# Optimization experiments

Measured on AMD Instinct MI355X. Metric: run time of the kernel, lower is better.

Reference implementation:

```python
import jax, jax.numpy as jnp
import numpy as np

B, S, D, H = 8, 2048, 256, 4
DH = D // H
DFF = 4 * D


def setup_inputs() -> dict:
    key = jax.random.key(0)
    ks = jax.random.split(key, 32)
    w = lambda k, sh: (jax.random.normal(k, sh, jnp.float32) * 0.02)
    inp = {
        'global_feat': jax.random.normal(ks[0], (B, S, D), jnp.float32),
        'local_feat': jax.random.normal(ks[1], (B, S, D), jnp.float32),
        'text_feat': jax.random.normal(ks[2], (B, S, D), jnp.float32),
        'Wl1': w(ks[3], (D, D)), 'bl1': jnp.zeros((D,), jnp.float32),
        'Wl2': w(ks[4], (D, D)), 'bl2': jnp.zeros((D,), jnp.float32),
        'Wg': w(ks[5], (D, D)), 'bg': jnp.zeros((D,), jnp.float32),
        'Wgq': w(ks[6], (D, D)), 'bgq': jnp.zeros((D,), jnp.float32),
        'Wgk': w(ks[7], (D, D)), 'bgk': jnp.zeros((D,), jnp.float32),
        'Wgv': w(ks[8], (D, D)), 'bgv': jnp.zeros((D,), jnp.float32),
        'Wpq': w(ks[9], (D, D)), 'bpq': jnp.zeros((D,), jnp.float32),
        'Wpk': w(ks[10], (D, D)), 'bpk': jnp.zeros((D,), jnp.float32),
        'Wpv': w(ks[11], (D, D)), 'bpv': jnp.zeros((D,), jnp.float32),
        'Wd': w(ks[12], (D, D)), 'bd': jnp.zeros((D,), jnp.float32),
        'Wm1': w(ks[13], (D, DFF)), 'bm1': jnp.zeros((DFF,), jnp.float32),
        'Wm2': w(ks[14], (DFF, D)), 'bm2': jnp.zeros((D,), jnp.float32),
        'Wml': w(ks[15], (D, D)), 'bml': jnp.zeros((D,), jnp.float32),
    }
    return inp


def _heads(x):
    # [B,S,D] -> [B,H,S,DH]
    return x.reshape(B, S, H, DH).transpose(0, 2, 1, 3)


def _merge(x):
    # [B,H,S,DH] -> [B,S,D]
    return x.transpose(0, 2, 1, 3).reshape(B, S, D)


def reference(global_feat, local_feat, text_feat,
              Wl1, bl1, Wl2, bl2, Wg, bg,
              Wgq, bgq, Wgk, bgk, Wgv, bgv,
              Wpq, bpq, Wpk, bpk, Wpv, bpv,
              Wd, bd, Wm1, bm1, Wm2, bm2, Wml, bml):
    scale = 1.0 / jnp.sqrt(jnp.asarray(DH, jnp.float32))
    # embedding projections (dropout inactive in eval mode)
    dup_local = local_feat @ Wl1 + bl1      # local_embedding_1
    local = local_feat @ Wl2 + bl2          # local_embedding_2
    glob = global_feat @ Wg + bg            # global_embedding
    # global branch: Q from global, K/V from local
    gq = _heads(glob @ Wgq + bgq)
    gk = _heads(local @ Wgk + bgk)
    gv = _heads(local @ Wgv + bgv)
    # local branch: Q from duplicate local, K/V from text
    pq = _heads(dup_local @ Wpq + bpq)
    pk = _heads(text_feat @ Wpk + bpk)
    pv = _heads(text_feat @ Wpv + bpv)
    glb_probs = jax.nn.softmax(jnp.einsum('bhqd,bhkd->bhqk', gq, gk) * scale, axis=-1)
    plb_probs = jax.nn.softmax(jnp.einsum('bhqd,bhkd->bhqk', pq, pk) * scale, axis=-1)
    # bridging matmul: fuse probability maps
    plb_enhanced = jnp.einsum('bhqk,bhkl->bhql', glb_probs, plb_probs)
    glb_ctx = _merge(jnp.einsum('bhqk,bhkd->bhqd', glb_probs, gv))
    plb_ctx = _merge(jnp.einsum('bhqk,bhkd->bhqd', plb_enhanced, pv))
    out = (glb_ctx + plb_ctx) @ Wd + bd
    # GPT-style MLP (c_fc -> GELU -> c_proj)
    out = jax.nn.gelu(out @ Wm1 + bm1) @ Wm2 + bm2
    out = out @ Wml + bml
    return out
```

## Files before the change

kernel.cpp:

```cpp
#include <hip/hip_runtime.h>
#include <math.h>

#define Bn 8
#define Sn 2048
#define Dn 256
#define Hn 4
#define DHn 64
#define Mn (Bn*Sn)

typedef short bf16x8 __attribute__((ext_vector_type(8)));
typedef float f32x2  __attribute__((ext_vector_type(2)));
typedef float f32x4  __attribute__((ext_vector_type(4)));
typedef float f32x16 __attribute__((ext_vector_type(16)));
typedef int   i32x4  __attribute__((ext_vector_type(4)));
typedef unsigned short u16;
typedef unsigned int   u32;
typedef unsigned long long u64;

#if defined(__has_builtin)
#if __has_builtin(__builtin_amdgcn_global_load_lds)
#define HAVE_GLL 1
#endif
#if __has_builtin(__builtin_amdgcn_permlane32_swap)
#define HAVE_PLS 1
#endif
#endif
#ifndef HAVE_GLL
#define HAVE_GLL 0
#endif
#ifndef HAVE_PLS
#define HAVE_PLS 0
#endif

__device__ __forceinline__ u16 f2b(float f){
    u32 u = __float_as_uint(f);
    u32 r = (u + 0x7fffu + ((u >> 16) & 1u)) >> 16;
    return (u16)r;
}
__device__ __forceinline__ float b2f(u16 h){ return __uint_as_float(((u32)h) << 16); }
__device__ __forceinline__ u32 cvtpk(float lo, float hi){
    u32 r;
    asm("v_cvt_pk_bf16_f32 %0, %1, %2" : "=v"(r) : "v"(lo), "v"(hi));
    return r;
}

__device__ __forceinline__ float gelu_f(float x){
    const float K1 = 2.3021143113f;
    const float K2 = 0.1029390163f;
    float x2 = x * x;
    float arg = fmaf(x2 * x, K2, x * K1);
    float e = exp2f(arg);
    float r = __builtin_amdgcn_rcpf(e + 1.0f);
    return x - x * r;
}

struct WtArgs {
    const float* src[13];
    int kdim[13], ndim[13], dstoff[13], t0[13], rm[13];
};
struct BcArgs {
    const float* W2[4];
    const float* b1[4];
    const float* b2[4];
    int off[4];
    float* fb;
    int bc0;
};

__global__ __launch_bounds__(256) void prep_k(const float* __restrict__ lf, const float* __restrict__ gf,
                                              const float* __restrict__ tf,
                                              u16* __restrict__ o0, u16* __restrict__ o1, u16* __restrict__ o2,
                                              WtArgs a, u16* __restrict__ dst, BcArgs bc)
{
    __shared__ float tile[32][33];
    int bx = blockIdx.x;
    if (bx < 6144){
        int part = bx >> 11, blk = bx & 2047;
        const float* s = (part == 0) ? lf : (part == 1) ? gf : tf;
        u16* d = (part == 0) ? o0 : (part == 1) ? o1 : o2;
        size_t base = ((size_t)blk * 256 + threadIdx.x) * 8;
        float4 v0 = *(const float4*)(s + base);
        float4 v1 = *(const float4*)(s + base + 4);
        i32x4 o;
        o[0] = (int)cvtpk(v0.x, v0.y); o[1] = (int)cvtpk(v0.z, v0.w);
        o[2] = (int)cvtpk(v1.x, v1.y); o[3] = (int)cvtpk(v1.z, v1.w);
        *(i32x4*)(d + base) = o;
        return;
    }
    if (bx >= bc.bc0){
        int p = bx - bc.bc0, aa = threadIdx.x;
        const float* W2 = bc.W2[p];
        const float* b1 = bc.b1[p];
        const float* b2 = bc.b2[p];
        float s = b2[aa];
        for (int j = 0; j < 256; ++j) s = fmaf(b1[j], W2[(size_t)j*256 + aa], s);
        bc.fb[bc.off[p] + aa] = s;
        if (p == 0) bc.fb[1024 + aa] = 0.f;
        return;
    }
    int tb = bx - 6144;
    int wi = 0;
    #pragma unroll
    for (int i = 1; i < 13; ++i) if (tb >= a.t0[i]) wi = i;
    int tt = tb - a.t0[wi];
    int N = a.ndim[wi], K = a.kdim[wi];
    int ntn = N >> 5;
    int tn = tt % ntn, tk = tt / ntn;
    int n0 = tn * 32, k0 = tk * 32;
    const float* src = a.src[wi];
    u16* out = dst + a.dstoff[wi];
    int r = threadIdx.x >> 5, c = threadIdx.x & 31;
    if (a.rm[wi]){
        #pragma unroll
        for (int rr = 0; rr < 4; ++rr){
            size_t idx = (size_t)(k0 + r*4 + rr) * N + n0 + c;
            out[idx] = f2b(src[idx]);
        }
        return;
    }
    #pragma unroll
    for (int rr = 0; rr < 4; ++rr)
        tile[r*4+rr][c] = src[(size_t)(k0 + r*4 + rr) * N + n0 + c];
    __syncthreads();
    #pragma unroll
    for (int rr = 0; rr < 4; ++rr)
        out[(size_t)(n0 + r*4 + rr) * K + k0 + c] = f2b(tile[c][r*4+rr]);
}

struct Grp {
    const u16* A[6];
    const u16* Wt[6];
    const float* bias[6];
    void* C[6];
    float scale[6];
};

template<int ACT, int OUTF32>
__global__ __launch_bounds__(256, 4) void gemm_k(Grp g, int N, int K)
{
    const u32 gx = gridDim.x, gy = gridDim.y;
    const u32 lgx = (u32)__builtin_ctz(gx);
    const u32 lgy = (u32)__builtin_ctz(gy);
    const u32 total = gx * gy * gridDim.z;
    const u32 lid = (blockIdx.z * gy + blockIdx.y) * gx + blockIdx.x;
    const u32 nl = (lid & 7) * (total >> 3) + (lid >> 3);
    const u32 bz = nl >> (lgx + lgy);
    const u32 by = (nl >> lgx) & (gy - 1);
    const u32 bx = nl & (gx - 1);

    const u16* __restrict__ A   = g.A[bz];
    const u16* __restrict__ Wt  = g.Wt[bz];
    const float* __restrict__ bias = g.bias[bz];
    void* __restrict__ Cv = g.C[bz];
    const float scale = g.scale[bz];

    __shared__ u16 sm[2][6144];
    const int tid = threadIdx.x;
    const int w = tid >> 6, lane = tid & 63;
    const int l15 = lane & 15, l4 = lane >> 4;
    const int wr = w & 1, wc = w >> 1;
    const int bm = by << 6, bn = bx << 7;
    const int xq = l4 ^ ((lane >> 1) & 3);

    f32x4 acc[4][2];
    #pragma unroll
    for (int nf = 0; nf < 4; ++nf)
        #pragma unroll
        for (int mf = 0; mf < 2; ++mf){
            acc[nf][mf][0]=0.f; acc[nf][mf][1]=0.f; acc[nf][mf][2]=0.f; acc[nf][mf][3]=0.f;
        }

    auto STAGE = [&](int buf, int kt){
        #pragma unroll
        for (int j = 0; j < 3; ++j){
            int ch = w*192 + j*64 + lane;
            int isB = ch >= 256;
            int cc  = isB ? ch - 256 : ch;
            int row = cc >> 2, q = cc & 3;
            int qs  = q ^ ((row >> 1) & 3);
            const u16* src = isB ? (Wt + (size_t)(bn + row) * K + kt + qs*8)
                                 : (A  + (size_t)(bm + row) * K + kt + qs*8);
#if HAVE_GLL
            u16* lb = &sm[buf][(size_t)(w*192 + j*64) * 8];
            __builtin_amdgcn_global_load_lds((const __attribute__((address_space(1))) void*)src,
                                             (__attribute__((address_space(3))) void*)lb, 16, 0, 0);
#else
            *(i32x4*)&sm[buf][(size_t)ch * 8] = *(const i32x4*)src;
#endif
        }
    };

    STAGE(0, 0);
    const int nk = K >> 5;
    for (int t = 0; t < nk; ++t){
        const int cur = t & 1;
        if (t + 1 < nk){
            STAGE(cur ^ 1, (t + 1) << 5);
#if HAVE_GLL
            asm volatile("s_waitcnt vmcnt(3)" ::: "memory");
#endif
        } else {
#if HAVE_GLL
            asm volatile("s_waitcnt vmcnt(0)" ::: "memory");
#endif
        }
        __builtin_amdgcn_s_barrier();
        asm volatile("" ::: "memory");

        const u16* As = sm[cur];
        const u16* Bs = sm[cur] + 2048;
        bf16x8 wf[4], af[2];
        #pragma unroll
        for (int nf = 0; nf < 4; ++nf)
            wf[nf] = *(const bf16x8*)(Bs + (size_t)(wc*64 + nf*16 + l15) * 32 + xq*8);
        #pragma unroll
        for (int mf = 0; mf < 2; ++mf)
            af[mf] = *(const bf16x8*)(As + (size_t)(wr*32 + mf*16 + l15) * 32 + xq*8);
        __builtin_amdgcn_s_setprio(1);
        #pragma unroll
        for (int nf = 0; nf < 4; ++nf)
            #pragma unroll
            for (int mf = 0; mf < 2; ++mf)
                acc[nf][mf] = __builtin_amdgcn_mfma_f32_16x16x32_bf16(wf[nf], af[mf], acc[nf][mf], 0, 0, 0);
        __builtin_amdgcn_s_setprio(0);

        asm volatile("" ::: "memory");
        __builtin_amdgcn_s_barrier();
    }

    #pragma unroll
    for (int nf = 0; nf < 4; ++nf){
        const int n0 = bn + wc*64 + nf*16 + l4*4;
        float4 b4 = *(const float4*)(bias + n0);
        #pragma unroll
        for (int mf = 0; mf < 2; ++mf){
            const int m = bm + wr*32 + mf*16 + l15;
            float r0 = (acc[nf][mf][0] + b4.x) * scale;
            float r1 = (acc[nf][mf][1] + b4.y) * scale;
            float r2 = (acc[nf][mf][2] + b4.z) * scale;
            float r3 = (acc[nf][mf][3] + b4.w) * scale;
            if (ACT){ r0 = gelu_f(r0); r1 = gelu_f(r1); r2 = gelu_f(r2); r3 = gelu_f(r3); }
            if (OUTF32){
                float4 o; o.x = r0; o.y = r1; o.z = r2; o.w = r3;
                *(float4*)((float*)Cv + (size_t)m * N + n0) = o;
            } else {
                u64 p = (u64)cvtpk(r0, r1) | ((u64)cvtpk(r2, r3) << 32);
                *(u64*)((u16*)Cv + (size_t)m * N + n0) = p;
            }
        }
    }
}

template<int FUSE>
__global__ __launch_bounds__(512, 2) void attn_k(const u16* __restrict__ Q, const u16* __restrict__ Kp,
                                                 const u16* __restrict__ Vp, u16* __restrict__ O,
                                                 const u16* __restrict__ ADD)
{
    __shared__ u16 Kl[2][4608];
    __shared__ u16 Vt[2][4608];

    const int tid = threadIdx.x;
    const int w = tid >> 6, lane = tid & 63;
    const int c31 = lane & 31, h = lane >> 5;

    const int lid = blockIdx.x;
    const int nl = (lid & 7) * 32 + (lid >> 3);
    const int bh = nl >> 3;
    const int qb = (nl & 7) << 8;
    const size_t hb = (size_t)(bh >> 2) * Sn * Dn + (size_t)(bh & 3) * DHn;
    const int qrow = qb + w*32 + c31;

    bf16x8 qf[4];
    #pragma unroll
    for (int kc = 0; kc < 4; ++kc)
        qf[kc] = *(const bf16x8*)(Q + hb + (size_t)qrow * Dn + kc*16 + h*8);

    f32x16 ot0, ot1;
    #pragma unroll
    for (int r = 0; r < 16; ++r){ ot0[r] = 0.f; ot1[r] = 0.f; }
    float ll = 0.f;

    int koff0[4], koff1[4];
    #pragma unroll
    for (int kc = 0; kc < 4; ++kc){
        koff0[kc] = c31*72        + kc*16 + h*8;
        koff1[kc] = (32 + c31)*72 + kc*16 + h*8;
    }

    const int isK = tid >= 256;
    const int t2 = tid & 255;
    const int krow = t2 >> 2, kq = t2 & 3;
    const int vk0 = (t2 & 15) * 4, vd0 = (t2 >> 4) * 4;
    const u32 SEL_LO = 0x05040100u, SEL_HI = 0x07060302u;

    i32x4 kr0, kr1;
    u64 v0, v1, v2, v3;
    auto LOADKV = [&](int kt2){
        if (isK){
            const u16* kb = Kp + hb + (size_t)(kt2 + krow) * Dn + kq*8;
            kr0 = *(const i32x4*)kb;
            kr1 = *(const i32x4*)(kb + 32);
        } else {
            const u16* vb = Vp + hb + (size_t)(kt2 + vk0) * Dn + vd0;
            v0 = *(const u64*)(vb);
            v1 = *(const u64*)(vb + Dn);
            v2 = *(const u64*)(vb + 2*Dn);
            v3 = *(const u64*)(vb + 3*Dn);
        }
    };
    auto WRITEKV = [&](int buf){
        if (isK){
            *(i32x4*)&Kl[buf][(size_t)krow*72 + kq*8]      = kr0;
            *(i32x4*)&Kl[buf][(size_t)krow*72 + kq*8 + 32] = kr1;
        } else {
            u32 a0 = (u32)v0, a1 = (u32)v1, a2 = (u32)v2, a3 = (u32)v3;
            u32 b0 = (u32)(v0 >> 32), b1 = (u32)(v1 >> 32), b2 = (u32)(v2 >> 32), b3 = (u32)(v3 >> 32);
            u64 wd0 = (u64)__builtin_amdgcn_perm(a1, a0, SEL_LO) | ((u64)__builtin_amdgcn_perm(a3, a2, SEL_LO) << 32);
            u64 wd1 = (u64)__builtin_amdgcn_perm(a1, a0, SEL_HI) | ((u64)__builtin_amdgcn_perm(a3, a2, SEL_HI) << 32);
            u64 wd2 = (u64)__builtin_amdgcn_perm(b1, b0, SEL_LO) | ((u64)__builtin_amdgcn_perm(b3, b2, SEL_LO) << 32);
            u64 wd3 = (u64)__builtin_amdgcn_perm(b1, b0, SEL_HI) | ((u64)__builtin_amdgcn_perm(b3, b2, SEL_HI) << 32);
            *(u64*)&Vt[buf][(size_t)(vd0 + 0)*72 + vk0] = wd0;
            *(u64*)&Vt[buf][(size_t)(vd0 + 1)*72 + vk0] = wd1;
            *(u64*)&Vt[buf][(size_t)(vd0 + 2)*72 + vk0] = wd2;
            *(u64*)&Vt[buf][(size_t)(vd0 + 3)*72 + vk0] = wd3;
        }
    };

    LOADKV(0);
    WRITEKV(0);
    __syncthreads();

    #pragma unroll 2
    for (int t = 0; t < 32; ++t){
        const int c = t & 1;
        const bool more = (t < 31);
        if (more) LOADKV((t + 1) << 6);

        f32x16 s0, s1;
        #pragma unroll
        for (int r = 0; r < 16; ++r){ s0[r] = 0.f; s1[r] = 0.f; }
        __builtin_amdgcn_s_setprio(1);
        #pragma unroll
        for (int kc = 0; kc < 4; ++kc){
            bf16x8 k0 = *(const bf16x8*)&Kl[c][koff0[kc]];
            bf16x8 k1 = *(const bf16x8*)&Kl[c][koff1[kc]];
            s0 = __builtin_amdgcn_mfma_f32_32x32x16_bf16(k0, qf[kc], s0, 0, 0, 0);
            s1 = __builtin_amdgcn_mfma_f32_32x32x16_bf16(k1, qf[kc], s1, 0, 0, 0);
        }
        __builtin_amdgcn_s_setprio(0);

        f32x2 pp0[8], pp1[8];
        f32x2 rv = {0.f, 0.f};
        #pragma unroll
        for (int r = 0; r < 8; ++r){
            pp0[r][0] = exp2f(s0[2*r]); pp0[r][1] = exp2f(s0[2*r+1]);
            pp1[r][0] = exp2f(s1[2*r]); pp1[r][1] = exp2f(s1[2*r+1]);
            rv += pp0[r];
            rv += pp1[r];
        }
        ll += rv[0] + rv[1];

        __builtin_amdgcn_s_setprio(1);
        #pragma unroll
        for (int kc = 0; kc < 4; ++kc){
            const int iA = 2*kc, iB = 2*kc + 1;
            u32 wA0, wA1, wB0, wB1;
            if (kc < 2){
                wA0 = cvtpk(pp0[iA*2+0][0], pp0[iA*2+0][1]);
                wA1 = cvtpk(pp0[iA*2+1][0], pp0[iA*2+1][1]);
                wB0 = cvtpk(pp0[iB*2+0][0], pp0[iB*2+0][1]);
                wB1 = cvtpk(pp0[iB*2+1][0], pp0[iB*2+1][1]);
            } else {
                wA0 = cvtpk(pp1[(iA-4)*2+0][0], pp1[(iA-4)*2+0][1]);
                wA1 = cvtpk(pp1[(iA-4)*2+1][0], pp1[(iA-4)*2+1][1]);
                wB0 = cvtpk(pp1[(iB-4)*2+0][0], pp1[(iB-4)*2+0][1]);
                wB1 = cvtpk(pp1[(iB-4)*2+1][0], pp1[(iB-4)*2+1][1]);
            }
            i32x4 pw;
#if HAVE_PLS
            {
                auto r02 = __builtin_amdgcn_permlane32_swap((int)wA0, (int)wB0, false, false);
                auto r13 = __builtin_amdgcn_permlane32_swap((int)wA1, (int)wB1, false, false);
                pw[0] = r02[0]; pw[1] = r13[0]; pw[2] = r02[1]; pw[3] = r13[1];
            }
#else
            {
                u32 s0v = h ? wA0 : wB0, s1v = h ? wA1 : wB1;
                u32 g0 = (u32)__shfl_xor((int)s0v, 32);
                u32 g1 = (u32)__shfl_xor((int)s1v, 32);
                pw[0] = (int)(h ? g0 : wA0);
                pw[1] = (int)(h ? g1 : wA1);
                pw[2] = (int)(h ? wB0 : g0);
                pw[3] = (int)(h ? wB1 : g1);
            }
#endif
            bf16x8 pb = *(bf16x8*)&pw;
            bf16x8 va  = *(const bf16x8*)&Vt[c][koff0[kc]];
            bf16x8 vb2 = *(const bf16x8*)&Vt[c][koff1[kc]];
            ot0 = __builtin_amdgcn_mfma_f32_32x32x16_bf16(va,  pb, ot0, 0, 0, 0);
            ot1 = __builtin_amdgcn_mfma_f32_32x32x16_bf16(vb2, pb, ot1, 0, 0, 0);
        }
        __builtin_amdgcn_s_setprio(0);

        if (more) WRITEKV(c ^ 1);
        __syncthreads();
    }

    ll += __shfl_xor(ll, 32);
    float inv = 1.0f / ll;
    #pragma unroll
    for (int rg = 0; rg < 4; ++rg){
        int d0 = 8*rg + 4*h;
        float r0 = ot0[4*rg+0]*inv, r1 = ot0[4*rg+1]*inv, r2 = ot0[4*rg+2]*inv, r3 = ot0[4*rg+3]*inv;
        float x0 = ot1[4*rg+0]*inv, x1 = ot1[4*rg+1]*inv, x2 = ot1[4*rg+2]*inv, x3 = ot1[4*rg+3]*inv;
        if (FUSE){
            u64 ga = *(const u64*)&ADD[hb + (size_t)qrow * Dn + d0];
            u64 gb = *(const u64*)&ADD[hb + (size_t)qrow * Dn + 32 + d0];
            r0 += b2f((u16)ga);         r1 += b2f((u16)(ga >> 16));
            r2 += b2f((u16)(ga >> 32)); r3 += b2f((u16)(ga >> 48));
            x0 += b2f((u16)gb);         x1 += b2f((u16)(gb >> 16));
            x2 += b2f((u16)(gb >> 32)); x3 += b2f((u16)(gb >> 48));
        }
        *(u64*)&O[hb + (size_t)qrow * Dn + d0]      = (u64)cvtpk(r0, r1) | ((u64)cvtpk(r2, r3) << 32);
        *(u64*)&O[hb + (size_t)qrow * Dn + 32 + d0] = (u64)cvtpk(x0, x1) | ((u64)cvtpk(x2, x3) << 32);
    }
}

extern "C" void kernel_launch(void* const* d_in, const int* in_sizes, int n_in,
                              void* d_out, int out_size, void* d_ws, size_t ws_size,
                              hipStream_t stream)
{
    (void)in_sizes; (void)n_in; (void)out_size; (void)ws_size;

    const float* gf  = (const float*)d_in[0];
    const float* lf  = (const float*)d_in[1];
    const float* tf  = (const float*)d_in[2];
    const float* Wl1 = (const float*)d_in[3];  const float* bl1 = (const float*)d_in[4];
    const float* Wl2 = (const float*)d_in[5];  const float* bl2 = (const float*)d_in[6];
    const float* Wg  = (const float*)d_in[7];  const float* bg  = (const float*)d_in[8];
    const float* Wgq = (const float*)d_in[9];  const float* bgq = (const float*)d_in[10];
    const float* Wgk = (const float*)d_in[11]; const float* bgk = (const float*)d_in[12];
    const float* Wgv = (const float*)d_in[13]; const float* bgv = (const float*)d_in[14];
    const float* Wpq = (const float*)d_in[15]; const float* bpq = (const float*)d_in[16];
    const float* bpk = (const float*)d_in[18];
    const float* bpv = (const float*)d_in[20];
    const float* bd  = (const float*)d_in[22];
    const float* bm1 = (const float*)d_in[24];
    const float* bm2 = (const float*)d_in[26];
    const float* Wml = (const float*)d_in[27]; const float* bml = (const float*)d_in[28];

    const float C1 = 0.18033688011112042f;

    u16* ws = (u16*)d_ws;
    const size_t U = (size_t)Mn * Dn;
    u16* S[9];
    for (int i = 0; i < 9; ++i) S[i] = ws + (size_t)i * U;
    u16* wtb = ws + 9 * U;

    const int sq = 65536;
    u16* Wpqt = wtb + 0*sq;  u16* Wgqt = wtb + 1*sq;  u16* Wgkt = wtb + 2*sq;  u16* Wgvt = wtb + 3*sq;
    u16* Wpkt = wtb + 4*sq;  u16* Wpvt = wtb + 5*sq;  u16* Wdt  = wtb + 6*sq;  u16* Wmlt = wtb + 7*sq;
    u16* Wm1t  = wtb + 524288;
    u16* Wm2t  = wtb + 786432;
    u16* Wl1rm = wtb + 1048576;
    u16* Wl2rm = wtb + 1114112;
    u16* Wgrm  = wtb + 1179648;
    u16* Wcpqt = wtb + 1245184;
    u16* Wcgqt = wtb + 1310720;
    u16* Wcgkt = wtb + 1376256;
    u16* Wcgvt = wtb + 1441792;
    float* fb  = (float*)(wtb + 1507328);

    WtArgs wa;
    const float* wsrc[13] = {Wpq, Wgq, Wgk, Wgv, (const float*)d_in[17], (const float*)d_in[19],
                             (const float*)d_in[21], Wml,
                             (const float*)d_in[23], (const float*)d_in[25], Wl1, Wl2, Wg};
    const int wdst[13] = {0, sq, 2*sq, 3*sq, 4*sq, 5*sq, 6*sq, 7*sq, 524288, 786432,
                          1048576, 1114112, 1179648};
    for (int i = 0; i < 13; ++i){
        wa.src[i] = wsrc[i];
        wa.kdim[i] = 256; wa.ndim[i] = 256;
        wa.dstoff[i] = wdst[i];
        wa.rm[i] = (i >= 10);
    }
    wa.ndim[8] = 1024;
    wa.kdim[9] = 1024;
    int acc_t = 0;
    for (int i = 0; i < 13; ++i){
        wa.t0[i] = acc_t;
        acc_t += (wa.ndim[i] >> 5) * (wa.kdim[i] >> 5);
    }
    BcArgs bc;
    bc.W2[0] = Wpq; bc.W2[1] = Wgq; bc.W2[2] = Wgk; bc.W2[3] = Wgv;
    bc.b1[0] = bl1; bc.b1[1] = bg;  bc.b1[2] = bl2; bc.b1[3] = bl2;
    bc.b2[0] = bpq; bc.b2[1] = bgq; bc.b2[2] = bgk; bc.b2[3] = bgv;
    bc.off[0] = 0; bc.off[1] = 256; bc.off[2] = 512; bc.off[3] = 768;
    bc.fb = fb; bc.bc0 = 6144 + acc_t;
    prep_k<<<dim3(6144 + acc_t + 4), 256, 0, stream>>>(lf, gf, tf, S[0], S[1], S[2], wa, wtb, bc);

    auto GN = [&](const Grp& g, int ng, int M, int N, int K, int act, int of32){
        dim3 gr(N / 128, M / 64, ng);
        if (act)        gemm_k<1,0><<<gr, 256, 0, stream>>>(g, N, K);
        else if (of32)  gemm_k<0,1><<<gr, 256, 0, stream>>>(g, N, K);
        else            gemm_k<0,0><<<gr, 256, 0, stream>>>(g, N, K);
    };
    auto G1 = [&](const u16* A, const u16* Wt_, const float* b, void* C, int M, int N, int K,
                  float sc, int act, int of32){
        Grp g{};
        g.A[0] = A; g.Wt[0] = Wt_; g.bias[0] = b; g.C[0] = C; g.scale[0] = sc;
        GN(g, 1, M, N, K, act, of32);
    };

    {
        Grp g{};
        g.A[0] = Wpqt; g.Wt[0] = Wl1rm; g.bias[0] = fb + 1024; g.C[0] = Wcpqt; g.scale[0] = 1.f;
        g.A[1] = Wgqt; g.Wt[1] = Wgrm;  g.bias[1] = fb + 1024; g.C[1] = Wcgqt; g.scale[1] = 1.f;
        g.A[2] = Wgkt; g.Wt[2] = Wl2rm; g.bias[2] = fb + 1024; g.C[2] = Wcgkt; g.scale[2] = 1.f;
        g.A[3] = Wgvt; g.Wt[3] = Wl2rm; g.bias[3] = fb + 1024; g.C[3] = Wcgvt; g.scale[3] = 1.f;
        GN(g, 4, 256, 256, 256, 0, 0);
    }

    {
        Grp g{};
        g.A[0] = S[0]; g.Wt[0] = Wcpqt; g.bias[0] = fb + 0;   g.C[0] = S[3]; g.scale[0] = C1;
        g.A[1] = S[1]; g.Wt[1] = Wcgqt; g.bias[1] = fb + 256; g.C[1] = S[6]; g.scale[1] = C1;
        g.A[2] = S[0]; g.Wt[2] = Wcgkt; g.bias[2] = fb + 512; g.C[2] = S[7]; g.scale[2] = 1.f;
        g.A[3] = S[0]; g.Wt[3] = Wcgvt; g.bias[3] = fb + 768; g.C[3] = S[8]; g.scale[3] = 1.f;
        g.A[4] = S[2]; g.Wt[4] = Wpkt;  g.bias[4] = bpk;      g.C[4] = S[4]; g.scale[4] = 1.f;
        g.A[5] = S[2]; g.Wt[5] = Wpvt;  g.bias[5] = bpv;      g.C[5] = S[5]; g.scale[5] = 1.f;
        GN(g, 6, Mn, 256, 256, 0, 0);
    }

    attn_k<1><<<dim3(256), 512, 0, stream>>>(S[3], S[4], S[5], S[0], S[8]);
    attn_k<0><<<dim3(256), 512, 0, stream>>>(S[6], S[7], S[0], S[1], nullptr);

    G1(S[1], Wdt,  bd,  S[2],  Mn, 256,  256,  1.f, 0, 0);
    G1(S[2], Wm1t, bm1, S[3],  Mn, 1024, 256,  1.f, 1, 0);
    G1(S[3], Wm2t, bm2, S[7],  Mn, 256,  1024, 1.f, 0, 0);
    G1(S[7], Wmlt, bml, d_out, Mn, 256,  256,  1.f, 0, 1);
}
```

Before: 240.4 us.

## Fuse fp32-to-bf16 input conversion into projection GEMM and retile attention blocks

Drops the separate fp32-to-bf16 conversion of the three input tensors from the prep kernel. A new grouped GEMM reads the fp32 activations directly and converts them while staging into LDS, which removes a full write and re-read of the converted inputs. The attention kernel is also reorganized from 512-thread blocks over 256 queries to 256-thread blocks over 128 queries, with each thread loading both K and V for 128-key tiles that are split into two 64-key halves. This doubles the grid size, but every block now streams the full K/V sequence, so total K/V traffic increases.

```diff
diff --git a/kernel.cpp b/kernel.cpp
--- a/kernel.cpp
+++ b/kernel.cpp
@@ -67,26 +67,10 @@
     int bc0;
 };
 
-__global__ __launch_bounds__(256) void prep_k(const float* __restrict__ lf, const float* __restrict__ gf,
-                                              const float* __restrict__ tf,
-                                              u16* __restrict__ o0, u16* __restrict__ o1, u16* __restrict__ o2,
-                                              WtArgs a, u16* __restrict__ dst, BcArgs bc)
+__global__ __launch_bounds__(256) void prep_k(WtArgs a, u16* __restrict__ dst, BcArgs bc)
 {
     __shared__ float tile[32][33];
     int bx = blockIdx.x;
-    if (bx < 6144){
-        int part = bx >> 11, blk = bx & 2047;
-        const float* s = (part == 0) ? lf : (part == 1) ? gf : tf;
-        u16* d = (part == 0) ? o0 : (part == 1) ? o1 : o2;
-        size_t base = ((size_t)blk * 256 + threadIdx.x) * 8;
-        float4 v0 = *(const float4*)(s + base);
-        float4 v1 = *(const float4*)(s + base + 4);
-        i32x4 o;
-        o[0] = (int)cvtpk(v0.x, v0.y); o[1] = (int)cvtpk(v0.z, v0.w);
-        o[2] = (int)cvtpk(v1.x, v1.y); o[3] = (int)cvtpk(v1.z, v1.w);
-        *(i32x4*)(d + base) = o;
-        return;
-    }
     if (bx >= bc.bc0){
         int p = bx - bc.bc0, aa = threadIdx.x;
         const float* W2 = bc.W2[p];
@@ -98,7 +82,7 @@
         if (p == 0) bc.fb[1024 + aa] = 0.f;
         return;
     }
-    int tb = bx - 6144;
+    int tb = bx;
     int wi = 0;
     #pragma unroll
     for (int i = 1; i < 13; ++i) if (tb >= a.t0[i]) wi = i;
@@ -251,22 +235,157 @@
     }
 }
 
+struct Grp32 {
+    const float* A[6];
+    const u16* Wt[6];
+    const float* bias[6];
+    void* C[6];
+    float scale[6];
+};
+
+__global__ __launch_bounds__(256, 4) void gemm32_k(Grp32 g, int N, int K)
+{
+    const u32 gx = gridDim.x, gy = gridDim.y;
+    const u32 lgx = (u32)__builtin_ctz(gx);
+    const u32 lgy = (u32)__builtin_ctz(gy);
+    const u32 total = gx * gy * gridDim.z;
+    const u32 lid = (blockIdx.z * gy + blockIdx.y) * gx + blockIdx.x;
+    const u32 nl = (lid & 7) * (total >> 3) + (lid >> 3);
+    const u32 bz = nl >> (lgx + lgy);
+    const u32 by = (nl >> lgx) & (gy - 1);
+    const u32 bx = nl & (gx - 1);
+
+    const float* __restrict__ A = g.A[bz];
+    const u16* __restrict__ Wt  = g.Wt[bz];
+    const float* __restrict__ bias = g.bias[bz];
+    void* __restrict__ Cv = g.C[bz];
+    const float scale = g.scale[bz];
+
+    __shared__ u16 sm[2][6144];
+    const int tid = threadIdx.x;
+    const int w = tid >> 6, lane = tid & 63;
+    const int l15 = lane & 15, l4 = lane >> 4;
+    const int wr = w & 1, wc = w >> 1;
+    const int bm = by << 6, bn = bx << 7;
+    const int xq = l4 ^ ((lane >> 1) & 3);
+
+    f32x4 acc[4][2];
+    #pragma unroll
+    for (int nf = 0; nf < 4; ++nf)
+        #pragma unroll
+        for (int mf = 0; mf < 2; ++mf){
+            acc[nf][mf][0]=0.f; acc[nf][mf][1]=0.f; acc[nf][mf][2]=0.f; acc[nf][mf][3]=0.f;
+        }
+
+    const int arow = tid >> 2, aq = tid & 3;
+    const int aqs = aq ^ ((arow >> 1) & 3);
+    const float* Ab = A + (size_t)(bm + arow) * K + aqs*8;
+    float4 a0r, a1r;
+    auto A_ISSUE = [&](int kt){
+        a0r = *(const float4*)(Ab + kt);
+        a1r = *(const float4*)(Ab + kt + 4);
+    };
+    auto A_WRITE = [&](int buf){
+        i32x4 o;
+        o[0] = (int)cvtpk(a0r.x, a0r.y); o[1] = (int)cvtpk(a0r.z, a0r.w);
+        o[2] = (int)cvtpk(a1r.x, a1r.y); o[3] = (int)cvtpk(a1r.z, a1r.w);
+        *(i32x4*)&sm[buf][(size_t)tid * 8] = o;
+    };
+    auto B_STAGE = [&](int buf, int kt){
+        #pragma unroll
+        for (int j = 0; j < 2; ++j){
+            int ch = w*128 + j*64 + lane;
+            int row = ch >> 2, q = ch & 3;
+            int qs  = q ^ ((row >> 1) & 3);
+            const u16* src = Wt + (size_t)(bn + row) * K + kt + qs*8;
+#if HAVE_GLL
+            u16* lb = &sm[buf][2048 + (size_t)(w*128 + j*64) * 8];
+            __builtin_amdgcn_global_load_lds((const __attribute__((address_space(1))) void*)src,
+                                             (__attribute__((address_space(3))) void*)lb, 16, 0, 0);
+#else
+            *(i32x4*)&sm[buf][2048 + (size_t)ch * 8] = *(const i32x4*)src;
+#endif
+        }
+    };
+
+    A_ISSUE(0);
+    B_STAGE(0, 0);
+    A_WRITE(0);
+    __syncthreads();
+
+    const int nk = K >> 5;
+    for (int t = 0; t < nk; ++t){
+        const int cur = t & 1;
+        if (t + 1 < nk){
+            A_ISSUE((t + 1) << 5);
+            B_STAGE(cur ^ 1, (t + 1) << 5);
+#if HAVE_GLL
+            asm volatile("s_waitcnt vmcnt(4)" ::: "memory");
+#endif
+        } else {
+#if HAVE_GLL
+            asm volatile("s_waitcnt vmcnt(0)" ::: "memory");
+#endif
+        }
+        __builtin_amdgcn_s_barrier();
+        asm volatile("" ::: "memory");
+
+        const u16* As = sm[cur];
+        const u16* Bs = sm[cur] + 2048;
+        bf16x8 wf[4], af[2];
+        #pragma unroll
+        for (int nf = 0; nf < 4; ++nf)
+            wf[nf] = *(const bf16x8*)(Bs + (size_t)(wc*64 + nf*16 + l15) * 32 + xq*8);
+        #pragma unroll
+        for (int mf = 0; mf < 2; ++mf)
+            af[mf] = *(const bf16x8*)(As + (size_t)(wr*32 + mf*16 + l15) * 32 + xq*8);
+        __builtin_amdgcn_s_setprio(1);
+        #pragma unroll
+        for (int nf = 0; nf < 4; ++nf)
+            #pragma unroll
+            for (int mf = 0; mf < 2; ++mf)
+                acc[nf][mf] = __builtin_amdgcn_mfma_f32_16x16x32_bf16(wf[nf], af[mf], acc[nf][mf], 0, 0, 0);
+        __builtin_amdgcn_s_setprio(0);
+
+        if (t + 1 < nk) A_WRITE(cur ^ 1);
+        asm volatile("" ::: "memory");
+        asm volatile("s_waitcnt lgkmcnt(0)" ::: "memory");
+        __builtin_amdgcn_s_barrier();
+    }
+
+    #pragma unroll
+    for (int nf = 0; nf < 4; ++nf){
+        const int n0 = bn + wc*64 + nf*16 + l4*4;
+        float4 b4 = *(const float4*)(bias + n0);
+        #pragma unroll
+        for (int mf = 0; mf < 2; ++mf){
+            const int m = bm + wr*32 + mf*16 + l15;
+            float r0 = (acc[nf][mf][0] + b4.x) * scale;
+            float r1 = (acc[nf][mf][1] + b4.y) * scale;
+            float r2 = (acc[nf][mf][2] + b4.z) * scale;
+            float r3 = (acc[nf][mf][3] + b4.w) * scale;
+            u64 p = (u64)cvtpk(r0, r1) | ((u64)cvtpk(r2, r3) << 32);
+            *(u64*)((u16*)Cv + (size_t)m * N + n0) = p;
+        }
+    }
+}
+
 template<int FUSE>
-__global__ __launch_bounds__(512, 2) void attn_k(const u16* __restrict__ Q, const u16* __restrict__ Kp,
+__global__ __launch_bounds__(256, 2) void attn_k(const u16* __restrict__ Q, const u16* __restrict__ Kp,
                                                  const u16* __restrict__ Vp, u16* __restrict__ O,
                                                  const u16* __restrict__ ADD)
 {
-    __shared__ u16 Kl[2][4608];
-    __shared__ u16 Vt[2][4608];
+    __shared__ u16 Kl[2][2][4608];
+    __shared__ u16 Vt[2][2][4608];
 
     const int tid = threadIdx.x;
     const int w = tid >> 6, lane = tid & 63;
     const int c31 = lane & 31, h = lane >> 5;
 
     const int lid = blockIdx.x;
-    const int nl = (lid & 7) * 32 + (lid >> 3);
-    const int bh = nl >> 3;
-    const int qb = (nl & 7) << 8;
+    const int nl = (lid & 7) * 64 + (lid >> 3);
+    const int bh = nl >> 4;
+    const int qb = (nl & 15) << 7;
     const size_t hb = (size_t)(bh >> 2) * Sn * Dn + (size_t)(bh & 3) * DHn;
     const int qrow = qb + w*32 + c31;
 
@@ -287,42 +406,55 @@
         koff1[kc] = (32 + c31)*72 + kc*16 + h*8;
     }
 
-    const int isK = tid >= 256;
-    const int t2 = tid & 255;
-    const int krow = t2 >> 2, kq = t2 & 3;
-    const int vk0 = (t2 & 15) * 4, vd0 = (t2 >> 4) * 4;
+    const int krow = tid >> 1, kq = (tid & 1) * 8;
+    const int khalf = krow >> 6, krow63 = krow & 63;
+    const int vk0 = (tid & 31) * 4, vd0 = (tid >> 5) * 4;
+    const int vhalf = vk0 >> 6, vk63 = vk0 & 63;
     const u32 SEL_LO = 0x05040100u, SEL_HI = 0x07060302u;
 
-    i32x4 kr0, kr1;
-    u64 v0, v1, v2, v3;
+    i32x4 kr[4];
+    u64 va_[4], vb_[4];
     auto LOADKV = [&](int kt2){
-        if (isK){
-            const u16* kb = Kp + hb + (size_t)(kt2 + krow) * Dn + kq*8;
-            kr0 = *(const i32x4*)kb;
-            kr1 = *(const i32x4*)(kb + 32);
-        } else {
-            const u16* vb = Vp + hb + (size_t)(kt2 + vk0) * Dn + vd0;
-            v0 = *(const u64*)(vb);
-            v1 = *(const u64*)(vb + Dn);
-            v2 = *(const u64*)(vb + 2*Dn);
-            v3 = *(const u64*)(vb + 3*Dn);
-        }
+        const u16* kb = Kp + hb + (size_t)(kt2 + krow) * Dn + kq;
+        kr[0] = *(const i32x4*)(kb);
+        kr[1] = *(const i32x4*)(kb + 16);
+        kr[2] = *(const i32x4*)(kb + 32);
+        kr[3] = *(const i32x4*)(kb + 48);
+        const u16* vb = Vp + hb + (size_t)(kt2 + vk0) * Dn + vd0;
+        va_[0] = *(const u64*)(vb);             va_[1] = *(const u64*)(vb + Dn);
+        va_[2] = *(const u64*)(vb + 2*Dn);      va_[3] = *(const u64*)(vb + 3*Dn);
+        vb_[0] = *(const u64*)(vb + 32);        vb_[1] = *(const u64*)(vb + Dn + 32);
+        vb_[2] = *(const u64*)(vb + 2*Dn + 32); vb_[3] = *(const u64*)(vb + 3*Dn + 32);
     };
     auto WRITEKV = [&](int buf){
-        if (isK){
-            *(i32x4*)&Kl[buf][(size_t)krow*72 + kq*8]      = kr0;
-            *(i32x4*)&Kl[buf][(size_t)krow*72 + kq*8 + 32] = kr1;
-        } else {
-            u32 a0 = (u32)v0, a1 = (u32)v1, a2 = (u32)v2, a3 = (u32)v3;
-            u32 b0 = (u32)(v0 >> 32), b1 = (u32)(v1 >> 32), b2 = (u32)(v2 >> 32), b3 = (u32)(v3 >> 32);
+        u16* kd = &Kl[buf][khalf][(size_t)krow63*72 + kq];
+        *(i32x4*)(kd)      = kr[0];
+        *(i32x4*)(kd + 16) = kr[1];
+        *(i32x4*)(kd + 32) = kr[2];
+        *(i32x4*)(kd + 48) = kr[3];
+        {
+            u32 a0 = (u32)va_[0], a1 = (u32)va_[1], a2 = (u32)va_[2], a3 = (u32)va_[3];
+            u32 b0 = (u32)(va_[0] >> 32), b1 = (u32)(va_[1] >> 32), b2 = (u32)(va_[2] >> 32), b3 = (u32)(va_[3] >> 32);
             u64 wd0 = (u64)__builtin_amdgcn_perm(a1, a0, SEL_LO) | ((u64)__builtin_amdgcn_perm(a3, a2, SEL_LO) << 32);
             u64 wd1 = (u64)__builtin_amdgcn_perm(a1, a0, SEL_HI) | ((u64)__builtin_amdgcn_perm(a3, a2, SEL_HI) << 32);
             u64 wd2 = (u64)__builtin_amdgcn_perm(b1, b0, SEL_LO) | ((u64)__builtin_amdgcn_perm(b3, b2, SEL_LO) << 32);
             u64 wd3 = (u64)__builtin_amdgcn_perm(b1, b0, SEL_HI) | ((u64)__builtin_amdgcn_perm(b3, b2, SEL_HI) << 32);
-            *(u64*)&Vt[buf][(size_t)(vd0 + 0)*72 + vk0] = wd0;
-            *(u64*)&Vt[buf][(size_t)(vd0 + 1)*72 + vk0] = wd1;
-            *(u64*)&Vt[buf][(size_t)(vd0 + 2)*72 + vk0] = wd2;
-            *(u64*)&Vt[buf][(size_t)(vd0 + 3)*72 + vk0] = wd3;
+            *(u64*)&Vt[buf][vhalf][(size_t)(vd0 + 0)*72 + vk63] = wd0;
+            *(u64*)&Vt[buf][vhalf][(size_t)(vd0 + 1)*72 + vk63] = wd1;
+            *(u64*)&Vt[buf][vhalf][(size_t)(vd0 + 2)*72 + vk63] = wd2;
+            *(u64*)&Vt[buf][vhalf][(size_t)(vd0 + 3)*72 + vk63] = wd3;
+        }
+        {
+            u32 a0 = (u32)vb_[0], a1 = (u32)vb_[1], a2 = (u32)vb_[2], a3 = (u32)vb_[3];
+            u32 b0 = (u32)(vb_[0] >> 32), b1 = (u32)(vb_[1] >> 32), b2 = (u32)(vb_[2] >> 32), b3 = (u32)(vb_[3] >> 32);
+            u64 wd0 = (u64)__builtin_amdgcn_perm(a1, a0, SEL_LO) | ((u64)__builtin_amdgcn_perm(a3, a2, SEL_LO) << 32);
+            u64 wd1 = (u64)__builtin_amdgcn_perm(a1, a0, SEL_HI) | ((u64)__builtin_amdgcn_perm(a3, a2, SEL_HI) << 32);
+            u64 wd2 = (u64)__builtin_amdgcn_perm(b1, b0, SEL_LO) | ((u64)__builtin_amdgcn_perm(b3, b2, SEL_LO) << 32);
+            u64 wd3 = (u64)__builtin_amdgcn_perm(b1, b0, SEL_HI) | ((u64)__builtin_amdgcn_perm(b3, b2, SEL_HI) << 32);
+            *(u64*)&Vt[buf][vhalf][(size_t)(vd0 + 32)*72 + vk63] = wd0;
+            *(u64*)&Vt[buf][vhalf][(size_t)(vd0 + 33)*72 + vk63] = wd1;
+            *(u64*)&Vt[buf][vhalf][(size_t)(vd0 + 34)*72 + vk63] = wd2;
+            *(u64*)&Vt[buf][vhalf][(size_t)(vd0 + 35)*72 + vk63] = wd3;
         }
     };
 
@@ -330,77 +462,79 @@
     WRITEKV(0);
     __syncthreads();
 
-    #pragma unroll 2
-    for (int t = 0; t < 32; ++t){
+    for (int t = 0; t < 16; ++t){
         const int c = t & 1;
-        const bool more = (t < 31);
-        if (more) LOADKV((t + 1) << 6);
-
-        f32x16 s0, s1;
-        #pragma unroll
-        for (int r = 0; r < 16; ++r){ s0[r] = 0.f; s1[r] = 0.f; }
-        __builtin_amdgcn_s_setprio(1);
-        #pragma unroll
-        for (int kc = 0; kc < 4; ++kc){
-            bf16x8 k0 = *(const bf16x8*)&Kl[c][koff0[kc]];
-            bf16x8 k1 = *(const bf16x8*)&Kl[c][koff1[kc]];
-            s0 = __builtin_amdgcn_mfma_f32_32x32x16_bf16(k0, qf[kc], s0, 0, 0, 0);
-            s1 = __builtin_amdgcn_mfma_f32_32x32x16_bf16(k1, qf[kc], s1, 0, 0, 0);
-        }
-        __builtin_amdgcn_s_setprio(0);
-
-        f32x2 pp0[8], pp1[8];
-        f32x2 rv = {0.f, 0.f};
-        #pragma unroll
-        for (int r = 0; r < 8; ++r){
-            pp0[r][0] = exp2f(s0[2*r]); pp0[r][1] = exp2f(s0[2*r+1]);
-            pp1[r][0] = exp2f(s1[2*r]); pp1[r][1] = exp2f(s1[2*r+1]);
-            rv += pp0[r];
-            rv += pp1[r];
-        }
-        ll += rv[0] + rv[1];
-
-        __builtin_amdgcn_s_setprio(1);
-        #pragma unroll
-        for (int kc = 0; kc < 4; ++kc){
-            const int iA = 2*kc, iB = 2*kc + 1;
-            u32 wA0, wA1, wB0, wB1;
-            if (kc < 2){
-                wA0 = cvtpk(pp0[iA*2+0][0], pp0[iA*2+0][1]);
-                wA1 = cvtpk(pp0[iA*2+1][0], pp0[iA*2+1][1]);
-                wB0 = cvtpk(pp0[iB*2+0][0], pp0[iB*2+0][1]);
-                wB1 = cvtpk(pp0[iB*2+1][0], pp0[iB*2+1][1]);
-            } else {
-                wA0 = cvtpk(pp1[(iA-4)*2+0][0], pp1[(iA-4)*2+0][1]);
-                wA1 = cvtpk(pp1[(iA-4)*2+1][0], pp1[(iA-4)*2+1][1]);
-                wB0 = cvtpk(pp1[(iB-4)*2+0][0], pp1[(iB-4)*2+0][1]);
-                wB1 = cvtpk(pp1[(iB-4)*2+1][0], pp1[(iB-4)*2+1][1]);
+        const bool more = (t < 15);
+        if (more) LOADKV((t + 1) << 7);
+
+        #pragma unroll
+        for (int hh = 0; hh < 2; ++hh){
+            f32x16 s0, s1;
+            #pragma unroll
+            for (int r = 0; r < 16; ++r){ s0[r] = 0.f; s1[r] = 0.f; }
+            __builtin_amdgcn_s_setprio(1);
+            #pragma unroll
+            for (int kc = 0; kc < 4; ++kc){
+                bf16x8 k0 = *(const bf16x8*)&Kl[c][hh][koff0[kc]];
+                bf16x8 k1 = *(const bf16x8*)&Kl[c][hh][koff1[kc]];
+                s0 = __builtin_amdgcn_mfma_f32_32x32x16_bf16(k0, qf[kc], s0, 0, 0, 0);
+                s1 = __builtin_amdgcn_mfma_f32_32x32x16_bf16(k1, qf[kc], s1, 0, 0, 0);
             }
-            i32x4 pw;
+            __builtin_amdgcn_s_setprio(0);
+
+            f32x2 pp0[8], pp1[8];
+            f32x2 rv = {0.f, 0.f};
+            #pragma unroll
+            for (int r = 0; r < 8; ++r){
+                pp0[r][0] = exp2f(s0[2*r]); pp0[r][1] = exp2f(s0[2*r+1]);
+                pp1[r][0] = exp2f(s1[2*r]); pp1[r][1] = exp2f(s1[2*r+1]);
+                rv += pp0[r];
+                rv += pp1[r];
+            }
+            ll += rv[0] + rv[1];
+
+            __builtin_amdgcn_s_setprio(1);
+            #pragma unroll
+            for (int kc = 0; kc < 4; ++kc){
+                const int iA = 2*kc, iB = 2*kc + 1;
+                u32 wA0, wA1, wB0, wB1;
+                if (kc < 2){
+                    wA0 = cvtpk(pp0[iA*2+0][0], pp0[iA*2+0][1]);
+                    wA1 = cvtpk(pp0[iA*2+1][0], pp0[iA*2+1][1]);
+                    wB0 = cvtpk(pp0[iB*2+0][0], pp0[iB*2+0][1]);
+                    wB1 = cvtpk(pp0[iB*2+1][0], pp0[iB*2+1][1]);
+                } else {
+                    wA0 = cvtpk(pp1[(iA-4)*2+0][0], pp1[(iA-4)*2+0][1]);
+                    wA1 = cvtpk(pp1[(iA-4)*2+1][0], pp1[(iA-4)*2+1][1]);
+                    wB0 = cvtpk(pp1[(iB-4)*2+0][0], pp1[(iB-4)*2+0][1]);
+                    wB1 = cvtpk(pp1[(iB-4)*2+1][0], pp1[(iB-4)*2+1][1]);
+                }
+                i32x4 pw;
 #if HAVE_PLS
-            {
-                auto r02 = __builtin_amdgcn_permlane32_swap((int)wA0, (int)wB0, false, false);
-                auto r13 = __builtin_amdgcn_permlane32_swap((int)wA1, (int)wB1, false, false);
-                pw[0] = r02[0]; pw[1] = r13[0]; pw[2] = r02[1]; pw[3] = r13[1];
+                {
+                    auto r02 = __builtin_amdgcn_permlane32_swap((int)wA0, (int)wB0, false, false);
+                    auto r13 = __builtin_amdgcn_permlane32_swap((int)wA1, (int)wB1, false, false);
+                    pw[0] = r02[0]; pw[1] = r13[0]; pw[2] = r02[1]; pw[3] = r13[1];
+                }
+#else
+                {
+                    u32 s0v = h ? wA0 : wB0, s1v = h ? wA1 : wB1;
+                    u32 g0 = (u32)__shfl_xor((int)s0v, 32);
+                    u32 g1 = (u32)__shfl_xor((int)s1v, 32);
+                    pw[0] = (int)(h ? g0 : wA0);
+                    pw[1] = (int)(h ? g1 : wA1);
+                    pw[2] = (int)(h ? wB0 : g0);
+                    pw[3] = (int)(h ? wB1 : g1);
+                }
+#endif
+                bf16x8 pb = *(bf16x8*)&pw;
+                bf16x8 va  = *(const bf16x8*)&Vt[c][hh][koff0[kc]];
+                bf16x8 vb2 = *(const bf16x8*)&Vt[c][hh][koff1[kc]];
+                ot0 = __builtin_amdgcn_mfma_f32_32x32x16_bf16(va,  pb, ot0, 0, 0, 0);
+                ot1 = __builtin_amdgcn_mfma_f32_32x32x16_bf16(vb2, pb, ot1, 0, 0, 0);
             }
-#else
-            {
-                u32 s0v = h ? wA0 : wB0, s1v = h ? wA1 : wB1;
-                u32 g0 = (u32)__shfl_xor((int)s0v, 32);
-                u32 g1 = (u32)__shfl_xor((int)s1v, 32);
-                pw[0] = (int)(h ? g0 : wA0);
-                pw[1] = (int)(h ? g1 : wA1);
-                pw[2] = (int)(h ? wB0 : g0);
-                pw[3] = (int)(h ? wB1 : g1);
-            }
-#endif
-            bf16x8 pb = *(bf16x8*)&pw;
-            bf16x8 va  = *(const bf16x8*)&Vt[c][koff0[kc]];
-            bf16x8 vb2 = *(const bf16x8*)&Vt[c][koff1[kc]];
-            ot0 = __builtin_amdgcn_mfma_f32_32x32x16_bf16(va,  pb, ot0, 0, 0, 0);
-            ot1 = __builtin_amdgcn_mfma_f32_32x32x16_bf16(vb2, pb, ot1, 0, 0, 0);
-        }
-        __builtin_amdgcn_s_setprio(0);
+            __builtin_amdgcn_s_setprio(0);
+        }
 
         if (more) WRITEKV(c ^ 1);
         __syncthreads();
@@ -495,8 +629,8 @@
     bc.b1[0] = bl1; bc.b1[1] = bg;  bc.b1[2] = bl2; bc.b1[3] = bl2;
     bc.b2[0] = bpq; bc.b2[1] = bgq; bc.b2[2] = bgk; bc.b2[3] = bgv;
     bc.off[0] = 0; bc.off[1] = 256; bc.off[2] = 512; bc.off[3] = 768;
-    bc.fb = fb; bc.bc0 = 6144 + acc_t;
-    prep_k<<<dim3(6144 + acc_t + 4), 256, 0, stream>>>(lf, gf, tf, S[0], S[1], S[2], wa, wtb, bc);
+    bc.fb = fb; bc.bc0 = acc_t;
+    prep_k<<<dim3(acc_t + 4), 256, 0, stream>>>(wa, wtb, bc);
 
     auto GN = [&](const Grp& g, int ng, int M, int N, int K, int act, int of32){
         dim3 gr(N / 128, M / 64, ng);
@@ -521,18 +655,19 @@
     }
 
     {
-        Grp g{};
-        g.A[0] = S[0]; g.Wt[0] = Wcpqt; g.bias[0] = fb + 0;   g.C[0] = S[3]; g.scale[0] = C1;
-        g.A[1] = S[1]; g.Wt[1] = Wcgqt; g.bias[1] = fb + 256; g.C[1] = S[6]; g.scale[1] = C1;
-        g.A[2] = S[0]; g.Wt[2] = Wcgkt; g.bias[2] = fb + 512; g.C[2] = S[7]; g.scale[2] = 1.f;
-        g.A[3] = S[0]; g.Wt[3] = Wcgvt; g.bias[3] = fb + 768; g.C[3] = S[8]; g.scale[3] = 1.f;
-        g.A[4] = S[2]; g.Wt[4] = Wpkt;  g.bias[4] = bpk;      g.C[4] = S[4]; g.scale[4] = 1.f;
-        g.A[5] = S[2]; g.Wt[5] = Wpvt;  g.bias[5] = bpv;      g.C[5] = S[5]; g.scale[5] = 1.f;
-        GN(g, 6, Mn, 256, 256, 0, 0);
-    }
-
-    attn_k<1><<<dim3(256), 512, 0, stream>>>(S[3], S[4], S[5], S[0], S[8]);
-    attn_k<0><<<dim3(256), 512, 0, stream>>>(S[6], S[7], S[0], S[1], nullptr);
+        Grp32 g{};
+        g.A[0] = lf; g.Wt[0] = Wcpqt; g.bias[0] = fb + 0;   g.C[0] = S[3]; g.scale[0] = C1;
+        g.A[1] = gf; g.Wt[1] = Wcgqt; g.bias[1] = fb + 256; g.C[1] = S[6]; g.scale[1] = C1;
+        g.A[2] = lf; g.Wt[2] = Wcgkt; g.bias[2] = fb + 512; g.C[2] = S[7]; g.scale[2] = 1.f;
+        g.A[3] = lf; g.Wt[3] = Wcgvt; g.bias[3] = fb + 768; g.C[3] = S[8]; g.scale[3] = 1.f;
+        g.A[4] = tf; g.Wt[4] = Wpkt;  g.bias[4] = bpk;      g.C[4] = S[4]; g.scale[4] = 1.f;
+        g.A[5] = tf; g.Wt[5] = Wpvt;  g.bias[5] = bpv;      g.C[5] = S[5]; g.scale[5] = 1.f;
+        dim3 gr(2, Mn / 64, 6);
+        gemm32_k<<<gr, 256, 0, stream>>>(g, 256, 256);
+    }
+
+    attn_k<1><<<dim3(512), 256, 0, stream>>>(S[3], S[4], S[5], S[0], S[8]);
+    attn_k<0><<<dim3(512), 256, 0, stream>>>(S[6], S[7], S[0], S[1], nullptr);
 
     G1(S[1], Wdt,  bd,  S[2],  Mn, 256,  256,  1.f, 0, 0);
     G1(S[2], Wm1t, bm1, S[3],  Mn, 1024, 256,  1.f, 1, 0);
```

Result: faster. 232.7 us (-3.2%).
